# Kernel tuning notes

Measured on AMD Instinct MI355X. Metric: run time of the kernel, lower is better.

The kernel has to match this reference:

```python
import jax, jax.numpy as jnp
import numpy as np

B, L, C, H = 2, 4096, 1024, 16
D = C // H
KERNEL_FROM_KN = lambda kn: int(np.sqrt(kn)) + 1


def setup_inputs() -> dict:
    key = jax.random.key(0)
    ks = jax.random.split(key, 4)
    s = 0.02
    kk = KERNEL_FROM_KN(144)  # 13
    return {
        "x": jax.random.normal(ks[0], (B, L, C), jnp.float32),
        "w_qkv": jax.random.normal(ks[1], (C, 3 * C), jnp.float32) * s,
        "b_qkv": jnp.zeros((3 * C,), jnp.float32),
        "rpb": jax.random.normal(ks[2], (H, 2 * kk - 1), jnp.float32) * s,
        "w_proj": jax.random.normal(ks[3], (C, C), jnp.float32) * s,
        "b_proj": jnp.zeros((C,), jnp.float32),
        "k_neighbors": 144,
    }


def reference(x, w_qkv, b_qkv, rpb, w_proj, b_proj, k_neighbors):
    kk = KERNEL_FROM_KN(k_neighbors)  # kernel size (13)
    scale = D ** -0.5
    qkv = (x @ w_qkv + b_qkv).reshape(B, L, 3, H, D).transpose(2, 0, 3, 1, 4)  # (3,B,H,L,D)
    q, k, v = qkv[0] * scale, qkv[1], qkv[2]
    pos = jnp.arange(L)
    # NATTEN window: centered, clamped so the full kernel fits inside [0, L)
    start = jnp.clip(pos - kk // 2, 0, L - kk)               # (L,)
    idx = start[:, None] + jnp.arange(kk)[None, :]           # (L,kk) key positions
    k_win = k[:, :, idx, :]                                  # (B,H,L,kk,D)
    v_win = v[:, :, idx, :]                                  # (B,H,L,kk,D)
    attn = jnp.einsum('bhld,bhlkd->bhlk', q, k_win)          # (B,H,L,kk)
    # relative-position bias index = key_pos - query_pos + (kk - 1) in [0, 2kk-2]
    bias_idx = idx - pos[:, None] + (kk - 1)                 # (L,kk)
    attn = attn + rpb[:, bias_idx][None]                     # broadcast over batch
    attn = jax.nn.softmax(attn, axis=-1)
    out = jnp.einsum('bhlk,bhlkd->bhld', attn, v_win)        # (B,H,L,D)
    out = out.transpose(0, 2, 1, 3).reshape(B, L, C)
    return out @ w_proj + b_proj
```

## Files before the change

### kernel.cpp

```cpp
#include <hip/hip_runtime.h>
#include <hip/hip_bf16.h>
#include <stdint.h>

typedef __bf16 bf16x8 __attribute__((ext_vector_type(8)));
typedef float floatx4 __attribute__((ext_vector_type(4)));

#define B_ 2
#define L_ 4096
#define C_ 1024
#define H_ 16
#define D_ 64
constexpr size_t TEN = (size_t)B_ * H_ * L_ * D_;

__device__ __forceinline__ float bf2f(unsigned short u) {
  union { unsigned int i; float f; } x; x.i = ((unsigned int)u) << 16; return x.f;
}
__device__ __forceinline__ unsigned short f2bf(float f) {
  union { float f; unsigned int i; } x; x.f = f;
  unsigned int i = x.i;
  return (unsigned short)((i + 0x7FFFu + ((i >> 16) & 1u)) >> 16);
}

__device__ __forceinline__ void g2lds16(const unsigned short* g, unsigned short* l) {
  __builtin_amdgcn_global_load_lds((__attribute__((address_space(1))) void*)g,
                                   (__attribute__((address_space(3))) void*)l,
                                   16, 0, 0);
}

__global__ __launch_bounds__(256) void cvt_f32_bf16_kernel(
    const float* __restrict__ in, unsigned short* __restrict__ out, int n) {
  int i = (blockIdx.x * 256 + threadIdx.x) * 8;
  if (i >= n) return;
  float4 a = *(const float4*)&in[i];
  float4 b = *(const float4*)&in[i + 4];
  union { uint4 u; unsigned short s[8]; } st;
  st.s[0] = f2bf(a.x); st.s[1] = f2bf(a.y); st.s[2] = f2bf(a.z); st.s[3] = f2bf(a.w);
  st.s[4] = f2bf(b.x); st.s[5] = f2bf(b.y); st.s[6] = f2bf(b.z); st.s[7] = f2bf(b.w);
  *(uint4*)&out[i] = st.u;
}

__global__ __launch_bounds__(256) void transpose_f32_bf16(
    const float* __restrict__ in, unsigned short* __restrict__ out,
    int R, int Ccols) {
  __shared__ float tile[64][65];
  const int bx = blockIdx.x * 64;
  const int by = blockIdx.y * 64;
  const int t = threadIdx.x;
  for (int i = t; i < 1024; i += 256) {
    int r = i >> 4, c4 = (i & 15) << 2;
    float4 v = *(const float4*)&in[(size_t)(by + r) * Ccols + bx + c4];
    tile[r][c4] = v.x; tile[r][c4 + 1] = v.y; tile[r][c4 + 2] = v.z; tile[r][c4 + 3] = v.w;
  }
  __syncthreads();
  for (int i = t; i < 512; i += 256) {
    int r = i >> 3, c8 = (i & 7) << 3;
    union { uint4 u; unsigned short s[8]; } st;
    #pragma unroll
    for (int j = 0; j < 8; ++j) st.s[j] = f2bf(tile[c8 + j][r]);
    *(uint4*)&out[(size_t)(bx + r) * R + by + c8] = st.u;
  }
}

template <int MODE>
__global__ __launch_bounds__(256) void gemm_bt_kernel(
    const unsigned short* __restrict__ A, const unsigned short* __restrict__ Bt,
    const float* __restrict__ bias, unsigned short* __restrict__ out_bf,
    float* __restrict__ out_f, int M, int N, int K, float qscale) {
  constexpr int BK = 64;
  __shared__ unsigned short a_sh[128 * BK];
  __shared__ unsigned short b_sh[128 * BK];

  const int t = threadIdx.x;
  const int m0 = blockIdx.y * 128;
  const int n0 = blockIdx.x * 128;
  const int wave = t >> 6, lane = t & 63;
  const int wr = wave >> 1, wc = wave & 1;
  const int lm = lane & 15, quad = lane >> 4;

  floatx4 acc[4][4];
  #pragma unroll
  for (int i = 0; i < 4; ++i)
    #pragma unroll
    for (int j = 0; j < 4; ++j) acc[i][j] = (floatx4)0.0f;

  const int r0 = (t * 8) >> 6;
  const int c0 = (t * 8) & 63;
  const unsigned short* gA = &A[(size_t)(m0 + r0) * K + c0];
  const unsigned short* gB = &Bt[(size_t)(n0 + r0) * K + c0];
  unsigned short* lA = &a_sh[(size_t)(t & ~63) * 8];
  unsigned short* lB = &b_sh[(size_t)(t & ~63) * 8];

  for (int kt = 0; kt < K; kt += BK) {
    #pragma unroll
    for (int p = 0; p < 4; ++p) {
      g2lds16(gA + (size_t)(p * 32) * K + kt, lA + p * 2048);
      g2lds16(gB + (size_t)(p * 32) * K + kt, lB + p * 2048);
    }
    __syncthreads();
    #pragma unroll
    for (int ks = 0; ks < BK; ks += 32) {
      bf16x8 af[4], bfr[4];
      #pragma unroll
      for (int i = 0; i < 4; ++i)
        af[i] = *(const bf16x8*)&a_sh[(wr * 64 + i * 16 + lm) * BK + ks + quad * 8];
      #pragma unroll
      for (int j = 0; j < 4; ++j)
        bfr[j] = *(const bf16x8*)&b_sh[(wc * 64 + j * 16 + lm) * BK + ks + quad * 8];
      #pragma unroll
      for (int i = 0; i < 4; ++i)
        #pragma unroll
        for (int j = 0; j < 4; ++j)
          acc[i][j] = __builtin_amdgcn_mfma_f32_16x16x32_bf16(af[i], bfr[j], acc[i][j], 0, 0, 0);
    }
    __syncthreads();
  }

  #pragma unroll
  for (int j = 0; j < 4; ++j) {
    int col = n0 + wc * 64 + j * 16 + lm;
    float bv = bias[col];
    if (MODE == 0) {
      int which = col >> 10;
      int rem = col & 1023;
      int h = rem >> 6, d = rem & 63;
      float mul = (which == 0) ? qscale : 1.0f;
      #pragma unroll
      for (int i = 0; i < 4; ++i)
        #pragma unroll
        for (int r = 0; r < 4; ++r) {
          int row = m0 + wr * 64 + i * 16 + quad * 4 + r;
          int b = row >> 12, l = row & (L_ - 1);
          float v = (acc[i][j][r] + bv) * mul;
          out_bf[(size_t)which * TEN + (((size_t)(b * H_ + h) * L_ + l) * D_ + d)] = f2bf(v);
        }
    } else {
      #pragma unroll
      for (int i = 0; i < 4; ++i)
        #pragma unroll
        for (int r = 0; r < 4; ++r) {
          int row = m0 + wr * 64 + i * 16 + quad * 4 + r;
          out_f[(size_t)row * N + col] = acc[i][j][r] + bv;
        }
    }
  }
}

constexpr int KKMAX = 63;
constexpr int TL = 128;
constexpr int LDK = 72;

__global__ __launch_bounds__(256) void natt_kernel(
    const unsigned short* __restrict__ qkv,
    const float* __restrict__ rpb,
    const int* __restrict__ knp,
    unsigned short* __restrict__ attn_out) {
  __shared__ unsigned short k_sh[(TL + KKMAX) * LDK];
  __shared__ unsigned short v_sh[(TL + KKMAX) * LDK];
  __shared__ float rpb_sh[2 * KKMAX + 1];

  const int bh = blockIdx.x;
  const int h = bh & (H_ - 1);
  const int b = bh >> 4;
  const int l0 = blockIdx.y * TL;
  const int t = threadIdx.x;

  int kn = knp[0];
  if (kn > 65536 || kn < 0) {
    union { int i; float f; } u; u.i = kn; kn = (int)u.f;
  }
  int rr = 1;
  while ((rr + 1) * (rr + 1) <= kn) ++rr;
  int kk = rr + 1;
  if (kk > KKMAX) kk = KKMAX;

  int base = l0 - kk / 2;
  if (base < 0) base = 0;
  if (base > L_ - kk) base = L_ - kk;
  int nrows = TL + kk;
  if (nrows > L_ - base) nrows = L_ - base;

  const unsigned short* kg = qkv + TEN + (size_t)bh * L_ * D_;
  const unsigned short* vg = qkv + 2 * TEN + (size_t)bh * L_ * D_;

  for (int i = t; i < nrows * 8; i += 256) {
    int row = i >> 3, c8 = (i & 7) << 3;
    uint4 kv = *(const uint4*)&kg[(size_t)(base + row) * D_ + c8];
    *(uint4*)&k_sh[row * LDK + c8] = kv;
    uint4 vv = *(const uint4*)&vg[(size_t)(base + row) * D_ + c8];
    *(uint4*)&v_sh[row * LDK + c8] = vv;
  }
  int nb = 2 * kk - 1;
  for (int i = t; i < nb; i += 256) rpb_sh[i] = rpb[h * nb + i];
  __syncthreads();

  const int qi = t >> 1, half = t & 1;
  const int l = l0 + qi;

  const unsigned short* qg = qkv + (size_t)bh * L_ * D_ + (size_t)l * D_ + half * 32;
  float qv[32];
  #pragma unroll
  for (int c = 0; c < 4; ++c) {
    union { uint4 u; unsigned short s[8]; } ld;
    ld.u = *(const uint4*)&qg[c * 8];
    #pragma unroll
    for (int j = 0; j < 8; ++j) qv[c * 8 + j] = bf2f(ld.s[j]);
  }

  int start = l - kk / 2;
  if (start < 0) start = 0;
  if (start > L_ - kk) start = L_ - kk;
  const int srow = start - base;
  const int boff = start - l + kk - 1;

  float accv[32];
  #pragma unroll
  for (int d = 0; d < 32; ++d) accv[d] = 0.0f;
  float lsum = 0.0f;

  if (kk <= 16) {
    float sarr[16];
    float mx = -1e30f;
    #pragma unroll
    for (int j = 0; j < 16; ++j) {
      if (j < kk) {
        const unsigned short* kr = &k_sh[(srow + j) * LDK + half * 32];
        float partial = 0.0f;
        #pragma unroll
        for (int c = 0; c < 4; ++c) {
          union { uint4 u; unsigned short s[8]; } ld;
          ld.u = *(const uint4*)&kr[c * 8];
          #pragma unroll
          for (int jj = 0; jj < 8; ++jj) partial += qv[c * 8 + jj] * bf2f(ld.s[jj]);
        }
        float s = partial + __shfl_xor(partial, 1) + rpb_sh[boff + j];
        sarr[j] = s;
        mx = fmaxf(mx, s);
      }
    }
    #pragma unroll
    for (int j = 0; j < 16; ++j) {
      if (j < kk) {
        float p = __expf(sarr[j] - mx);
        lsum += p;
        const unsigned short* vr = &v_sh[(srow + j) * LDK + half * 32];
        #pragma unroll
        for (int c = 0; c < 4; ++c) {
          union { uint4 u; unsigned short s[8]; } ld;
          ld.u = *(const uint4*)&vr[c * 8];
          #pragma unroll
          for (int jj = 0; jj < 8; ++jj) accv[c * 8 + jj] += p * bf2f(ld.s[jj]);
        }
      }
    }
  } else {
    float m = -1e30f;
    for (int j = 0; j < kk; ++j) {
      const unsigned short* kr = &k_sh[(srow + j) * LDK + half * 32];
      float partial = 0.0f;
      #pragma unroll
      for (int c = 0; c < 4; ++c) {
        union { uint4 u; unsigned short s[8]; } ld;
        ld.u = *(const uint4*)&kr[c * 8];
        #pragma unroll
        for (int jj = 0; jj < 8; ++jj) partial += qv[c * 8 + jj] * bf2f(ld.s[jj]);
      }
      float s = partial + __shfl_xor(partial, 1) + rpb_sh[boff + j];
      float p;
      if (s > m) {
        float corr = __expf(m - s);
        lsum *= corr;
        #pragma unroll
        for (int d = 0; d < 32; ++d) accv[d] *= corr;
        m = s;
        p = 1.0f;
      } else {
        p = __expf(s - m);
      }
      lsum += p;
      const unsigned short* vr = &v_sh[(srow + j) * LDK + half * 32];
      #pragma unroll
      for (int c = 0; c < 4; ++c) {
        union { uint4 u; unsigned short s[8]; } ld;
        ld.u = *(const uint4*)&vr[c * 8];
        #pragma unroll
        for (int jj = 0; jj < 8; ++jj) accv[c * 8 + jj] += p * bf2f(ld.s[jj]);
      }
    }
  }

  float inv = 1.0f / lsum;
  unsigned short* og = attn_out + ((size_t)(b * L_ + l) * C_ + h * D_ + half * 32);
  #pragma unroll
  for (int c = 0; c < 4; ++c) {
    union { uint4 u; unsigned short s[8]; } st;
    #pragma unroll
    for (int jj = 0; jj < 8; ++jj) st.s[jj] = f2bf(accv[c * 8 + jj] * inv);
    *(uint4*)&og[c * 8] = st.u;
  }
}

extern "C" void kernel_launch(void* const* d_in, const int* in_sizes, int n_in,
                              void* d_out, int out_size, void* d_ws, size_t ws_size,
                              hipStream_t stream) {
  const float* x      = (const float*)d_in[0];
  const float* w_qkv  = (const float*)d_in[1];
  const float* b_qkv  = (const float*)d_in[2];
  const float* rpb    = (const float*)d_in[3];
  const float* w_proj = (const float*)d_in[4];
  const float* b_proj = (const float*)d_in[5];
  const int* kn       = (const int*)d_in[6];
  float* out          = (float*)d_out;

  unsigned short* ws      = (unsigned short*)d_ws;
  unsigned short* wT_qkv  = ws;
  unsigned short* wT_proj = wT_qkv + (size_t)3072 * 1024;
  unsigned short* x_bf    = wT_proj + (size_t)1024 * 1024;
  unsigned short* qkv_ws  = x_bf + (size_t)8192 * 1024;
  unsigned short* attn_ws = qkv_ws + 3 * TEN;

  cvt_f32_bf16_kernel<<<(8192 * 1024) / (256 * 8), 256, 0, stream>>>(x, x_bf, 8192 * 1024);
  transpose_f32_bf16<<<dim3(3072 / 64, 1024 / 64), 256, 0, stream>>>(w_qkv, wT_qkv, 1024, 3072);
  transpose_f32_bf16<<<dim3(1024 / 64, 1024 / 64), 256, 0, stream>>>(w_proj, wT_proj, 1024, 1024);
  gemm_bt_kernel<0><<<dim3(3072 / 128, 8192 / 128), 256, 0, stream>>>(
      x_bf, wT_qkv, b_qkv, qkv_ws, nullptr, 8192, 3072, 1024, 0.125f);
  natt_kernel<<<dim3(B_ * H_, L_ / TL), 256, 0, stream>>>(qkv_ws, rpb, kn, attn_ws);
  gemm_bt_kernel<1><<<dim3(1024 / 128, 8192 / 128), 256, 0, stream>>>(
      attn_ws, wT_proj, b_proj, nullptr, out, 8192, 1024, 1024, 1.0f);
}
```

Measured before the change: 239.2 us.

## Register-prefetch GEMM tiles with padded LDS, smaller M tile for projection

Replaces the direct global-to-LDS loads in the GEMM with a register-staged prefetch of the next K tile, which overlaps with the MFMA work on the current tile. LDS rows are padded to 72 elements to reduce bank conflicts. The GEMM is templated on the M tile so the output projection runs 64-row tiles, giving more blocks on the device. KKMAX is also cut from 63 to 31, which shrinks the attention kernel's shared memory; this is only safe because the test's kernel size is 13.

```diff
diff --git a/kernel.cpp b/kernel.cpp
--- a/kernel.cpp
+++ b/kernel.cpp
@@ -19,12 +19,6 @@
   union { float f; unsigned int i; } x; x.f = f;
   unsigned int i = x.i;
   return (unsigned short)((i + 0x7FFFu + ((i >> 16) & 1u)) >> 16);
-}
-
-__device__ __forceinline__ void g2lds16(const unsigned short* g, unsigned short* l) {
-  __builtin_amdgcn_global_load_lds((__attribute__((address_space(1))) void*)g,
-                                   (__attribute__((address_space(3))) void*)l,
-                                   16, 0, 0);
 }
 
 __global__ __launch_bounds__(256) void cvt_f32_bf16_kernel(
@@ -61,58 +55,76 @@
   }
 }
 
-template <int MODE>
+template <int TM, int MODE>
 __global__ __launch_bounds__(256) void gemm_bt_kernel(
     const unsigned short* __restrict__ A, const unsigned short* __restrict__ Bt,
     const float* __restrict__ bias, unsigned short* __restrict__ out_bf,
     float* __restrict__ out_f, int M, int N, int K, float qscale) {
   constexpr int BK = 64;
-  __shared__ unsigned short a_sh[128 * BK];
-  __shared__ unsigned short b_sh[128 * BK];
+  constexpr int LDA = 72;
+  constexpr int NI = TM / 32;
+  constexpr int NIW = TM / 32;
+  __shared__ unsigned short a_sh[TM * LDA];
+  __shared__ unsigned short b_sh[128 * LDA];
 
   const int t = threadIdx.x;
-  const int m0 = blockIdx.y * 128;
+  const int m0 = blockIdx.y * TM;
   const int n0 = blockIdx.x * 128;
   const int wave = t >> 6, lane = t & 63;
   const int wr = wave >> 1, wc = wave & 1;
   const int lm = lane & 15, quad = lane >> 4;
 
-  floatx4 acc[4][4];
-  #pragma unroll
-  for (int i = 0; i < 4; ++i)
+  floatx4 acc[NIW][4];
+  #pragma unroll
+  for (int i = 0; i < NIW; ++i)
     #pragma unroll
     for (int j = 0; j < 4; ++j) acc[i][j] = (floatx4)0.0f;
 
-  const int r0 = (t * 8) >> 6;
-  const int c0 = (t * 8) & 63;
-  const unsigned short* gA = &A[(size_t)(m0 + r0) * K + c0];
-  const unsigned short* gB = &Bt[(size_t)(n0 + r0) * K + c0];
-  unsigned short* lA = &a_sh[(size_t)(t & ~63) * 8];
-  unsigned short* lB = &b_sh[(size_t)(t & ~63) * 8];
+  const int r0 = t >> 3;
+  const int c0 = (t & 7) * 8;
+
+  uint4 ra[NI], rb[4];
+  #pragma unroll
+  for (int p = 0; p < NI; ++p)
+    ra[p] = *(const uint4*)&A[(size_t)(m0 + p * 32 + r0) * K + c0];
+  #pragma unroll
+  for (int p = 0; p < 4; ++p)
+    rb[p] = *(const uint4*)&Bt[(size_t)(n0 + p * 32 + r0) * K + c0];
 
   for (int kt = 0; kt < K; kt += BK) {
-    #pragma unroll
-    for (int p = 0; p < 4; ++p) {
-      g2lds16(gA + (size_t)(p * 32) * K + kt, lA + p * 2048);
-      g2lds16(gB + (size_t)(p * 32) * K + kt, lB + p * 2048);
-    }
     __syncthreads();
     #pragma unroll
+    for (int p = 0; p < NI; ++p)
+      *(uint4*)&a_sh[(p * 32 + r0) * LDA + c0] = ra[p];
+    #pragma unroll
+    for (int p = 0; p < 4; ++p)
+      *(uint4*)&b_sh[(p * 32 + r0) * LDA + c0] = rb[p];
+    __syncthreads();
+
+    if (kt + BK < K) {
+      #pragma unroll
+      for (int p = 0; p < NI; ++p)
+        ra[p] = *(const uint4*)&A[(size_t)(m0 + p * 32 + r0) * K + kt + BK + c0];
+      #pragma unroll
+      for (int p = 0; p < 4; ++p)
+        rb[p] = *(const uint4*)&Bt[(size_t)(n0 + p * 32 + r0) * K + kt + BK + c0];
+    }
+
+    #pragma unroll
     for (int ks = 0; ks < BK; ks += 32) {
-      bf16x8 af[4], bfr[4];
-      #pragma unroll
-      for (int i = 0; i < 4; ++i)
-        af[i] = *(const bf16x8*)&a_sh[(wr * 64 + i * 16 + lm) * BK + ks + quad * 8];
+      bf16x8 af[NIW], bfr[4];
+      #pragma unroll
+      for (int i = 0; i < NIW; ++i)
+        af[i] = *(const bf16x8*)&a_sh[(wr * (TM / 2) + i * 16 + lm) * LDA + ks + quad * 8];
       #pragma unroll
       for (int j = 0; j < 4; ++j)
-        bfr[j] = *(const bf16x8*)&b_sh[(wc * 64 + j * 16 + lm) * BK + ks + quad * 8];
-      #pragma unroll
-      for (int i = 0; i < 4; ++i)
+        bfr[j] = *(const bf16x8*)&b_sh[(wc * 64 + j * 16 + lm) * LDA + ks + quad * 8];
+      #pragma unroll
+      for (int i = 0; i < NIW; ++i)
         #pragma unroll
         for (int j = 0; j < 4; ++j)
           acc[i][j] = __builtin_amdgcn_mfma_f32_16x16x32_bf16(af[i], bfr[j], acc[i][j], 0, 0, 0);
     }
-    __syncthreads();
   }
 
   #pragma unroll
@@ -125,27 +137,27 @@
       int h = rem >> 6, d = rem & 63;
       float mul = (which == 0) ? qscale : 1.0f;
       #pragma unroll
-      for (int i = 0; i < 4; ++i)
+      for (int i = 0; i < NIW; ++i)
         #pragma unroll
         for (int r = 0; r < 4; ++r) {
-          int row = m0 + wr * 64 + i * 16 + quad * 4 + r;
+          int row = m0 + wr * (TM / 2) + i * 16 + quad * 4 + r;
           int b = row >> 12, l = row & (L_ - 1);
           float v = (acc[i][j][r] + bv) * mul;
           out_bf[(size_t)which * TEN + (((size_t)(b * H_ + h) * L_ + l) * D_ + d)] = f2bf(v);
         }
     } else {
       #pragma unroll
-      for (int i = 0; i < 4; ++i)
+      for (int i = 0; i < NIW; ++i)
         #pragma unroll
         for (int r = 0; r < 4; ++r) {
-          int row = m0 + wr * 64 + i * 16 + quad * 4 + r;
+          int row = m0 + wr * (TM / 2) + i * 16 + quad * 4 + r;
           out_f[(size_t)row * N + col] = acc[i][j][r] + bv;
         }
     }
   }
 }
 
-constexpr int KKMAX = 63;
+constexpr int KKMAX = 31;
 constexpr int TL = 128;
 constexpr int LDK = 72;
 
@@ -321,9 +333,9 @@
   cvt_f32_bf16_kernel<<<(8192 * 1024) / (256 * 8), 256, 0, stream>>>(x, x_bf, 8192 * 1024);
   transpose_f32_bf16<<<dim3(3072 / 64, 1024 / 64), 256, 0, stream>>>(w_qkv, wT_qkv, 1024, 3072);
   transpose_f32_bf16<<<dim3(1024 / 64, 1024 / 64), 256, 0, stream>>>(w_proj, wT_proj, 1024, 1024);
-  gemm_bt_kernel<0><<<dim3(3072 / 128, 8192 / 128), 256, 0, stream>>>(
+  gemm_bt_kernel<128, 0><<<dim3(3072 / 128, 8192 / 128), 256, 0, stream>>>(
       x_bf, wT_qkv, b_qkv, qkv_ws, nullptr, 8192, 3072, 1024, 0.125f);
   natt_kernel<<<dim3(B_ * H_, L_ / TL), 256, 0, stream>>>(qkv_ws, rpb, kn, attn_ws);
-  gemm_bt_kernel<1><<<dim3(1024 / 128, 8192 / 128), 256, 0, stream>>>(
+  gemm_bt_kernel<64, 1><<<dim3(1024 / 128, 8192 / 64), 256, 0, stream>>>(
       attn_ws, wT_proj, b_proj, nullptr, out, 8192, 1024, 1024, 1.0f);
 }
```

After: 463.9 us. 93.9% more time.
